# Kernel optimization log

Hardware: AMD Instinct MI355X
Metric: run time of the kernel (lower is better)

The kernel has to match this reference:

```python
import jax, jax.numpy as jnp
import numpy as np
import math

B, L = 2, 768
C, CS, CZ, H, NB = 256, 256, 64, 8, 4
HD = C // H  # 32


def _layernorm(x, g, b):
    mu = jnp.mean(x, -1, keepdims=True)
    var = jnp.var(x, -1, keepdims=True)
    return (x - mu) * jax.lax.rsqrt(var + 1e-5) * g + b


def _adaln(x, cond, g, beta, pw, pb):
    # x: [B,L,C], cond: [B,C] -> LN(x)*(1+scale)+shift
    ss = cond @ pw + pb  # [B, 2C]
    scale, shift = jnp.split(ss, 2, axis=-1)
    return _layernorm(x, g, beta) * (1.0 + scale[:, None, :]) + shift[:, None, :]


def _gelu(x):
    return jax.nn.gelu(x, approximate=False)  # torch nn.GELU default = exact erf


def _axis_angle_to_R(v):
    # Rodrigues: [...,3] -> [...,3,3]
    n = jnp.linalg.norm(v, axis=-1, keepdims=True)
    angle = n[..., None]  # [...,1,1]
    axis = v / (n + 1e-8)
    x, y, z = axis[..., 0], axis[..., 1], axis[..., 2]
    zero = jnp.zeros_like(x)
    K = jnp.stack([
        jnp.stack([zero, -z, y], -1),
        jnp.stack([z, zero, -x], -1),
        jnp.stack([-y, x, zero], -1),
    ], -2)
    eye = jnp.broadcast_to(jnp.eye(3, dtype=v.dtype), K.shape)
    return eye + jnp.sin(angle) * K + (1.0 - jnp.cos(angle)) * (K @ K)


def setup_inputs() -> dict:
    key = jax.random.key(0)
    ks = iter(jax.random.split(key, 64))
    nk = lambda: next(ks)
    w = lambda shape, s=0.02: jax.random.normal(nk(), shape, jnp.float32) * s
    return {
        'rots': jax.random.normal(nk(), (B, L, 3, 3), jnp.float32),
        'trans': jax.random.normal(nk(), (B, L, 3), jnp.float32),
        't': jax.random.uniform(nk(), (B,), jnp.float32),
        'single': jax.random.normal(nk(), (B, L, CS), jnp.float32),
        'pair': jax.random.normal(nk(), (B, L, L, CZ), jnp.float32),
        'frame_w': w((12, C)), 'frame_b': w((C,)),
        'single_w': w((CS, C)), 'single_b': w((C,)),
        'tw1': w((C, 4 * C)), 'tb1': w((4 * C,)),
        'tw2': w((4 * C, C)), 'tb2': w((C,)),
        'out_w': w((C, 6)), 'out_b': w((6,)),
        'ag1': jnp.ones((NB, C)), 'abeta1': jnp.zeros((NB, C)),
        'apw1': w((NB, C, 2 * C)), 'apb1': w((NB, 2 * C)),
        'wq': w((NB, C, C)), 'wk': w((NB, C, C)), 'wv': w((NB, C, C)),
        'pw': w((NB, CZ, H)),
        'wo': w((NB, C, C)), 'wob': w((NB, C)),
        'ag2': jnp.ones((NB, C)), 'abeta2': jnp.zeros((NB, C)),
        'apw2': w((NB, C, 2 * C)), 'apb2': w((NB, 2 * C)),
        'fw1': w((NB, C, 4 * C)), 'fb1': w((NB, 4 * C)),
        'fw2': w((NB, 4 * C, C)), 'fb2': w((NB, C)),
    }


def reference(rots, trans, t, single, pair, frame_w, frame_b, single_w, single_b,
              tw1, tb1, tw2, tb2, out_w, out_b, ag1, abeta1, apw1, apb1,
              wq, wk, wv, pw, wo, wob, ag2, abeta2, apw2, apb2,
              fw1, fb1, fw2, fb2):
    Bq, Lq = trans.shape[:2]
    # frame featurization + single conditioning
    frame_feat = jnp.concatenate([rots.reshape(Bq, Lq, 9), trans], -1)  # [B,L,12]
    h = frame_feat @ frame_w + frame_b + single @ single_w + single_b   # [B,L,C]
    # Fourier time embedding -> MLP
    half = C // 2
    freqs = jnp.exp(-math.log(10000.0) * jnp.arange(half, dtype=jnp.float32) / half)
    args = t[:, None] * freqs
    temb = jnp.concatenate([jnp.cos(args), jnp.sin(args)], -1)          # [B,C]
    time_cond = _gelu(temb @ tw1 + tb1) @ tw2 + tb2                     # [B,C]
    scale = 1.0 / math.sqrt(HD)
    for i in range(NB):
        hh = _adaln(h, time_cond, ag1[i], abeta1[i], apw1[i], apb1[i])
        q = (hh @ wq[i]).reshape(Bq, Lq, H, HD)
        k = (hh @ wk[i]).reshape(Bq, Lq, H, HD)
        v = (hh @ wv[i]).reshape(Bq, Lq, H, HD)
        logits = jnp.einsum('bihd,bjhd->bhij', q, k) * scale
        logits = logits + jnp.einsum('bijc,ch->bhij', pair, pw[i])      # pair bias
        attn = jax.nn.softmax(logits, -1)
        out = jnp.einsum('bhij,bjhd->bihd', attn, v).reshape(Bq, Lq, C)
        h = h + out @ wo[i] + wob[i]
        h2 = _adaln(h, time_cond, ag2[i], abeta2[i], apw2[i], apb2[i])
        h = h + _gelu(h2 @ fw1[i] + fb1[i]) @ fw2[i] + fb2[i]
    corr = h @ out_w + out_b                                            # [B,L,6]
    R_upd = _axis_angle_to_R(corr[..., :3])
    t_upd = corr[..., 3:]
    # compose: new_R = R @ R_upd, new_t = R @ t_upd + t
    new_rots = rots @ R_upd
    new_trans = jnp.einsum('blij,blj->bli', rots, t_upd) + trans
    return jnp.concatenate([new_rots.reshape(Bq, Lq, 9), new_trans], -1)  # [B,L,12]
```

## Files before the change

### kernel.cpp

```cpp
#include <hip/hip_runtime.h>
#include <math.h>

#define BB 2
#define LL 768
#define CC 256
#define CZ 64
#define NH 8
#define NBLK 4
#define HD 32
#define BL (BB*LL)

typedef unsigned short ushort_t;
typedef float f32x4 __attribute__((ext_vector_type(4)));
typedef __bf16 bf16x8 __attribute__((ext_vector_type(8)));

__device__ __forceinline__ float gelu_exact(float x) {
    return 0.5f * x * (1.0f + erff(x * 0.70710678118654752f));
}

__device__ __forceinline__ ushort_t f2bf(float f) {
    union { float f; unsigned u; } x; x.f = f;
    unsigned r = x.u + 0x7fffu + ((x.u >> 16) & 1u);
    return (ushort_t)(r >> 16);
}

__device__ __forceinline__ float bf2f(ushort_t u) {
    union { unsigned u; float f; } x; x.u = ((unsigned)u) << 16;
    return x.f;
}

__global__ __launch_bounds__(512) void k_time_pre(
        const float* __restrict__ t, float* __restrict__ temb,
        float* __restrict__ tmid, float* __restrict__ time_cond) {
    int tid = threadIdx.x;
    int b = tid >> 8, idx = tid & 255;
    int fi = idx & 127;
    float f = expf(-logf(10000.0f) * (float)fi / 128.0f);
    float a = t[b] * f;
    temb[b * 256 + idx] = (idx < 128) ? cosf(a) : sinf(a);
    #pragma unroll
    for (int e = 0; e < 4; ++e) tmid[tid + 512 * e] = 0.f;
    time_cond[tid] = 0.f;
}

__global__ __launch_bounds__(256) void k_time1(
        const float* __restrict__ temb, const float* __restrict__ tw1,
        float* __restrict__ tmid) {
    int kc = blockIdx.x, b = blockIdx.y;
    int tid = threadIdx.x;
    __shared__ float te[32];
    if (tid < 32) te[tid] = temb[b * 256 + kc * 32 + tid];
    __syncthreads();
    float acc[4] = {0.f, 0.f, 0.f, 0.f};
    #pragma unroll
    for (int k = 0; k < 32; ++k) {
        const float* wr = tw1 + (size_t)(kc * 32 + k) * 1024;
        float tv = te[k];
        #pragma unroll
        for (int m = 0; m < 4; ++m) acc[m] += tv * wr[tid + 256 * m];
    }
    #pragma unroll
    for (int m = 0; m < 4; ++m) atomicAdd(&tmid[b * 1024 + tid + 256 * m], acc[m]);
}

__global__ __launch_bounds__(512) void k_time_gelu(
        float* __restrict__ tmid, const float* __restrict__ tb1) {
    int tid = threadIdx.x;
    #pragma unroll
    for (int e = 0; e < 4; ++e) {
        int i = tid + 512 * e;
        tmid[i] = gelu_exact(tmid[i] + tb1[i & 1023]);
    }
}

__global__ __launch_bounds__(256) void k_time2(
        const float* __restrict__ tmid, const float* __restrict__ tw2,
        const float* __restrict__ tb2, float* __restrict__ time_cond) {
    int kc = blockIdx.x, b = blockIdx.y;
    int tid = threadIdx.x;
    __shared__ float mg[64];
    if (tid < 64) mg[tid] = tmid[b * 1024 + kc * 64 + tid];
    __syncthreads();
    float acc = (kc == 0) ? tb2[tid] : 0.f;
    #pragma unroll
    for (int k = 0; k < 64; ++k)
        acc += mg[k] * tw2[(size_t)(kc * 64 + k) * 256 + tid];
    atomicAdd(&time_cond[b * 256 + tid], acc);
}

__global__ __launch_bounds__(512) void k_ss(
        const float* __restrict__ tc,
        const float* __restrict__ apw1, const float* __restrict__ apb1,
        const float* __restrict__ apw2, const float* __restrict__ apb2,
        float* __restrict__ ss1, float* __restrict__ ss2) {
    int n = blockIdx.x, b = blockIdx.y, which = blockIdx.z;
    const float* apw = which ? apw2 : apw1;
    const float* apb = which ? apb2 : apb1;
    float* ss = which ? ss2 : ss1;
    __shared__ float tcl[256];
    int tid = threadIdx.x;
    if (tid < 256) tcl[tid] = tc[b * 256 + tid];
    __syncthreads();
    float acc = apb[n * 512 + tid];
    const float* w = apw + (size_t)n * 256 * 512 + tid;
    #pragma unroll 8
    for (int k = 0; k < 256; ++k) acc += tcl[k] * w[(size_t)k * 512];
    ss[(size_t)(n * BB + b) * 512 + tid] = acc;
}

__global__ __launch_bounds__(256) void k_init_h(
        const float* __restrict__ rots, const float* __restrict__ trans,
        const float* __restrict__ single,
        const float* __restrict__ frame_w, const float* __restrict__ frame_b,
        const float* __restrict__ single_w, const float* __restrict__ single_b,
        float* __restrict__ h) {
    int row = blockIdx.x;
    int tid = threadIdx.x;
    __shared__ float ff[12];
    __shared__ float sr[256];
    if (tid < 9) ff[tid] = rots[(size_t)row * 9 + tid];
    else if (tid < 12) ff[tid] = trans[(size_t)row * 3 + (tid - 9)];
    sr[tid] = single[(size_t)row * 256 + tid];
    __syncthreads();
    float acc = frame_b[tid] + single_b[tid];
    #pragma unroll
    for (int k = 0; k < 12; ++k) acc += ff[k] * frame_w[k * 256 + tid];
    #pragma unroll 8
    for (int k = 0; k < 256; ++k) acc += sr[k] * single_w[k * 256 + tid];
    h[(size_t)row * 256 + tid] = acc;
}

__global__ __launch_bounds__(256) void k_adaln(
        const float* __restrict__ h, const float* __restrict__ g,
        const float* __restrict__ beta, const float* __restrict__ ss,
        float* __restrict__ out) {
    int row = blockIdx.x;
    int b = row / LL;
    int tid = threadIdx.x;
    float x = h[(size_t)row * 256 + tid];
    float s = x, sq = x * x;
    #pragma unroll
    for (int off = 32; off > 0; off >>= 1) {
        s  += __shfl_down(s,  off, 64);
        sq += __shfl_down(sq, off, 64);
    }
    __shared__ float red[8];
    int wave = tid >> 6, lane = tid & 63;
    if (lane == 0) { red[wave] = s; red[4 + wave] = sq; }
    __syncthreads();
    if (tid == 0) {
        float ts = red[0] + red[1] + red[2] + red[3];
        float tq = red[4] + red[5] + red[6] + red[7];
        float mu = ts * (1.0f / 256.0f);
        float var = tq * (1.0f / 256.0f) - mu * mu;
        red[0] = mu;
        red[1] = rsqrtf(var + 1e-5f);
    }
    __syncthreads();
    float mu = red[0], inv = red[1];
    float ln = (x - mu) * inv * g[tid] + beta[tid];
    float scale = ss[b * 512 + tid];
    float shift = ss[b * 512 + 256 + tid];
    out[(size_t)row * 256 + tid] = ln * (1.0f + scale) + shift;
}

__global__ __launch_bounds__(256) void k_adaln_bf(
        const float* __restrict__ h, const float* __restrict__ g,
        const float* __restrict__ beta, const float* __restrict__ ss,
        ushort_t* __restrict__ out) {
    int row = blockIdx.x;
    int b = row / LL;
    int tid = threadIdx.x;
    float x = h[(size_t)row * 256 + tid];
    float s = x, sq = x * x;
    #pragma unroll
    for (int off = 32; off > 0; off >>= 1) {
        s  += __shfl_down(s,  off, 64);
        sq += __shfl_down(sq, off, 64);
    }
    __shared__ float red[8];
    int wave = tid >> 6, lane = tid & 63;
    if (lane == 0) { red[wave] = s; red[4 + wave] = sq; }
    __syncthreads();
    if (tid == 0) {
        float ts = red[0] + red[1] + red[2] + red[3];
        float tq = red[4] + red[5] + red[6] + red[7];
        float mu = ts * (1.0f / 256.0f);
        float var = tq * (1.0f / 256.0f) - mu * mu;
        red[0] = mu;
        red[1] = rsqrtf(var + 1e-5f);
    }
    __syncthreads();
    float mu = red[0], inv = red[1];
    float ln = (x - mu) * inv * g[tid] + beta[tid];
    float scale = ss[b * 512 + tid];
    float shift = ss[b * 512 + 256 + tid];
    out[(size_t)row * 256 + tid] = f2bf(ln * (1.0f + scale) + shift);
}

__global__ __launch_bounds__(256) void k_wt(
        const float* __restrict__ wq, const float* __restrict__ wk,
        const float* __restrict__ wv, const float* __restrict__ wo,
        const float* __restrict__ fw1, const float* __restrict__ fw2,
        ushort_t* __restrict__ wqkv_bt, ushort_t* __restrict__ wo_bt,
        ushort_t* __restrict__ fw1_bt, ushort_t* __restrict__ fw2_bt) {
    int type = blockIdx.z, nb = blockIdx.y, idx = blockIdx.x;
    int K, N; const float* src; ushort_t* dst;
    switch (type) {
        case 0: K = 256; N = 256;  src = wq  + (size_t)nb * 65536;  dst = wqkv_bt + (size_t)nb * 196608;           break;
        case 1: K = 256; N = 256;  src = wk  + (size_t)nb * 65536;  dst = wqkv_bt + (size_t)nb * 196608 + 65536;   break;
        case 2: K = 256; N = 256;  src = wv  + (size_t)nb * 65536;  dst = wqkv_bt + (size_t)nb * 196608 + 131072;  break;
        case 3: K = 256; N = 256;  src = wo  + (size_t)nb * 65536;  dst = wo_bt  + (size_t)nb * 65536;             break;
        case 4: K = 256; N = 1024; src = fw1 + (size_t)nb * 262144; dst = fw1_bt + (size_t)nb * 262144;            break;
        default:K = 1024; N = 256; src = fw2 + (size_t)nb * 262144; dst = fw2_bt + (size_t)nb * 262144;            break;
    }
    int tilesN = N >> 6;
    int tiles = (K >> 6) * tilesN;
    if (idx >= tiles) return;
    int k0 = (idx / tilesN) * 64, n0 = (idx % tilesN) * 64;
    __shared__ float lds[64][65];
    int tn = threadIdx.x & 63, tk = threadIdx.x >> 6;
    #pragma unroll
    for (int r = 0; r < 16; ++r) {
        int kk = tk + 4 * r;
        lds[kk][tn] = src[(size_t)(k0 + kk) * N + n0 + tn];
    }
    __syncthreads();
    #pragma unroll
    for (int r = 0; r < 16; ++r) {
        int nn = tk + 4 * r;
        dst[(size_t)(n0 + nn) * K + k0 + tn] = f2bf(lds[tn][nn]);
    }
}

template<int KSTEPS, int MODE>
__global__ __launch_bounds__(256) void k_mfma(
        const ushort_t* __restrict__ A, const ushort_t* __restrict__ Wt,
        const float* __restrict__ bias, const float* __restrict__ resid,
        float* __restrict__ outf, ushort_t* __restrict__ outb,
        ushort_t* __restrict__ qo, ushort_t* __restrict__ ko,
        ushort_t* __restrict__ vo) {
    const int K = KSTEPS * 32;
    int m0 = blockIdx.x * 64, n0 = blockIdx.y * 64;
    int t = threadIdx.x;
    int wave = t >> 6, lane = t & 63, quad = lane >> 4, l16 = lane & 15;
    const bf16x8* Ap = (const bf16x8*)(A + (size_t)(m0 + wave * 16 + l16) * K + quad * 8);
    const bf16x8* Wp = (const bf16x8*)(Wt + (size_t)(n0 + l16) * K + quad * 8);
    const int wstride = 2 * K;
    f32x4 acc[4];
    #pragma unroll
    for (int nt = 0; nt < 4; ++nt) acc[nt] = f32x4{0.f, 0.f, 0.f, 0.f};

    #pragma unroll
    for (int ks = 0; ks < KSTEPS; ++ks) {
        bf16x8 av = Ap[ks * 4];
        #pragma unroll
        for (int nt = 0; nt < 4; ++nt) {
            bf16x8 bv = Wp[nt * wstride + ks * 4];
            acc[nt] = __builtin_amdgcn_mfma_f32_16x16x32_bf16(av, bv, acc[nt], 0, 0, 0);
        }
    }

    int row_base = m0 + wave * 16 + quad * 4;
    #pragma unroll
    for (int nt = 0; nt < 4; ++nt) {
        int n = n0 + nt * 16 + l16;
        #pragma unroll
        for (int r = 0; r < 4; ++r) {
            int row = row_base + r;
            float val = acc[nt][r];
            if (MODE == 0) {
                if (n < 512) {
                    ushort_t* dst = (n < 256) ? qo : ko;
                    dst[(size_t)row * 256 + (n & 255)] = f2bf(val);
                } else {
                    int d = n & 31, hd = (n >> 5) & 7;
                    int bb = (row >= LL) ? 1 : 0;
                    int i = row - bb * LL;
                    vo[(((size_t)(bb * NH + hd)) * 32 + d) * LL + i] = f2bf(val);
                }
            } else if (MODE == 1) {
                val += bias[n] + resid[(size_t)row * 256 + n];
                outf[(size_t)row * 256 + n] = val;
            } else {
                val = gelu_exact(val + bias[n]);
                outb[(size_t)row * 1024 + n] = f2bf(val);
            }
        }
    }
}

template<int KSTEPS>
__global__ __launch_bounds__(256) void k_mfma32(
        const ushort_t* __restrict__ A, const ushort_t* __restrict__ Wt,
        const float* __restrict__ bias, const float* __restrict__ resid,
        float* __restrict__ outf) {
    const int K = KSTEPS * 32;
    int m0 = blockIdx.x * 32, n0 = blockIdx.y * 32;
    int t = threadIdx.x;
    int wave = t >> 6, lane = t & 63, quad = lane >> 4, l16 = lane & 15;
    int msub = wave & 1, nsub = wave >> 1;
    const bf16x8* Ap = (const bf16x8*)(A + (size_t)(m0 + msub * 16 + l16) * K + quad * 8);
    const bf16x8* Wp = (const bf16x8*)(Wt + (size_t)(n0 + nsub * 16 + l16) * K + quad * 8);
    f32x4 acc = {0.f, 0.f, 0.f, 0.f};
    #pragma unroll 8
    for (int ks = 0; ks < KSTEPS; ++ks)
        acc = __builtin_amdgcn_mfma_f32_16x16x32_bf16(Ap[ks * 4], Wp[ks * 4], acc, 0, 0, 0);
    int n = n0 + nsub * 16 + l16;
    int row0 = m0 + msub * 16 + quad * 4;
    float bv = bias[n];
    #pragma unroll
    for (int r = 0; r < 4; ++r) {
        int row = row0 + r;
        outf[(size_t)row * 256 + n] = acc[r] + bv + resid[(size_t)row * 256 + n];
    }
}

template<int NCOL, int KCH>
__global__ __launch_bounds__(256) void k_gemm4(
        const float* __restrict__ A, const float* __restrict__ W,
        const float* __restrict__ bias, const float* __restrict__ resid,
        float* __restrict__ out, int flags) {
    const int N = 256 * NCOL;
    const int K = 256 * KCH;
    int row0 = blockIdx.x * 4;
    int tid = threadIdx.x;
    __shared__ float a_s[4][256];
    float acc[4][NCOL];
    #pragma unroll
    for (int r = 0; r < 4; ++r)
        #pragma unroll
        for (int m = 0; m < NCOL; ++m) acc[r][m] = 0.f;

    for (int kc = 0; kc < KCH; ++kc) {
        if (kc) __syncthreads();
        {
            int r = tid >> 6, c4 = tid & 63;
            float4 av = reinterpret_cast<const float4*>(
                A + (size_t)(row0 + r) * K + kc * 256)[c4];
            *reinterpret_cast<float4*>(&a_s[r][c4 * 4]) = av;
        }
        __syncthreads();
        const float* Wp = W + (size_t)kc * 256 * N + tid;
        #pragma unroll 4
        for (int k = 0; k < 256; ++k) {
            float bv[NCOL];
            #pragma unroll
            for (int m = 0; m < NCOL; ++m) bv[m] = Wp[(size_t)k * N + 256 * m];
            #pragma unroll
            for (int r = 0; r < 4; ++r) {
                float a = a_s[r][k];
                #pragma unroll
                for (int m = 0; m < NCOL; ++m) acc[r][m] += a * bv[m];
            }
        }
    }
    #pragma unroll
    for (int r = 0; r < 4; ++r) {
        int row = row0 + r;
        #pragma unroll
        for (int m = 0; m < NCOL; ++m) {
            int col = tid + 256 * m;
            float v = acc[r][m];
            if (flags & 1) v += bias[col];
            if (flags & 2) v = gelu_exact(v);
            if (flags & 4) v += resid[(size_t)row * N + col];
            out[(size_t)row * N + col] = v;
        }
    }
}

__global__ __launch_bounds__(256) void k_gemm_qkv(
        const float* __restrict__ A,
        const float* __restrict__ Wq, const float* __restrict__ Wk,
        const float* __restrict__ Wv,
        float* __restrict__ q, float* __restrict__ k_,
        float* __restrict__ v) {
    int row0 = blockIdx.x * 4;
    int tid = threadIdx.x;
    __shared__ float a_s[4][256];
    {
        int r = tid >> 6, c4 = tid & 63;
        float4 av = reinterpret_cast<const float4*>(
            A + (size_t)(row0 + r) * 256)[c4];
        *reinterpret_cast<float4*>(&a_s[r][c4 * 4]) = av;
    }
    __syncthreads();
    float aq[4] = {0,0,0,0}, ak[4] = {0,0,0,0}, av_[4] = {0,0,0,0};
    #pragma unroll 4
    for (int k = 0; k < 256; ++k) {
        float wq_ = Wq[(size_t)k * 256 + tid];
        float wk_ = Wk[(size_t)k * 256 + tid];
        float wv_ = Wv[(size_t)k * 256 + tid];
        #pragma unroll
        for (int r = 0; r < 4; ++r) {
            float a = a_s[r][k];
            aq[r]  += a * wq_;
            ak[r]  += a * wk_;
            av_[r] += a * wv_;
        }
    }
    #pragma unroll
    for (int r = 0; r < 4; ++r) {
        size_t o = (size_t)(row0 + r) * 256 + tid;
        q[o] = aq[r]; k_[o] = ak[r]; v[o] = av_[r];
    }
}

__global__ __launch_bounds__(256) void k_pairbias(
        const float* __restrict__ pair, const float* __restrict__ pw,
        float* __restrict__ pb) {
    int row = blockIdx.x;
    int b = row / LL, i = row % LL;
    int t = threadIdx.x;
    int wave = t >> 6, lane = t & 63, quad = lane >> 4, l16 = lane & 15;

    bf16x8 Bhi[2][2], Blo[2][2];
    #pragma unroll
    for (int tt = 0; tt < 2; ++tt) {
        int nh = tt * 16 + l16;
        int n = nh >> 3, hh = nh & 7;
        #pragma unroll
        for (int ks = 0; ks < 2; ++ks) {
            #pragma unroll
            for (int e = 0; e < 8; ++e) {
                int c = ks * 32 + quad * 8 + e;
                float w = pw[n * 512 + c * 8 + hh];
                __bf16 hi = (__bf16)w;
                float lo = w - (float)hi;
                Bhi[tt][ks][e] = hi;
                Blo[tt][ks][e] = (__bf16)lo;
            }
        }
    }

    const float* prow = pair + (size_t)row * LL * CZ;
    for (int x = 0; x < 12; ++x) {
        int j0 = (wave + 4 * x) * 16;
        bf16x8 Ahi[2], Alo[2];
        #pragma unroll
        for (int ks = 0; ks < 2; ++ks) {
            const float4* src = reinterpret_cast<const float4*>(
                prow + (size_t)(j0 + l16) * CZ + ks * 32 + quad * 8);
            float4 v0 = src[0], v1 = src[1];
            float f[8] = {v0.x, v0.y, v0.z, v0.w, v1.x, v1.y, v1.z, v1.w};
            #pragma unroll
            for (int e = 0; e < 8; ++e) {
                __bf16 hi = (__bf16)f[e];
                Ahi[ks][e] = hi;
                Alo[ks][e] = (__bf16)(f[e] - (float)hi);
            }
        }
        #pragma unroll
        for (int tt = 0; tt < 2; ++tt) {
            f32x4 acc = {0.f, 0.f, 0.f, 0.f};
            #pragma unroll
            for (int ks = 0; ks < 2; ++ks) {
                acc = __builtin_amdgcn_mfma_f32_16x16x32_bf16(Ahi[ks], Bhi[tt][ks], acc, 0, 0, 0);
                acc = __builtin_amdgcn_mfma_f32_16x16x32_bf16(Alo[ks], Bhi[tt][ks], acc, 0, 0, 0);
                acc = __builtin_amdgcn_mfma_f32_16x16x32_bf16(Ahi[ks], Blo[tt][ks], acc, 0, 0, 0);
            }
            int nh = tt * 16 + l16;
            float4 o = make_float4(acc[0], acc[1], acc[2], acc[3]);
            *reinterpret_cast<float4*>(
                pb + (((size_t)(b * 32 + nh)) * LL + i) * LL + j0 + quad * 4) = o;
        }
    }
}

__global__ __launch_bounds__(256) void k_attn_mfma(
        const ushort_t* __restrict__ qb, const ushort_t* __restrict__ kb,
        const ushort_t* __restrict__ vt, const float* __restrict__ pb,
        int n, ushort_t* __restrict__ outp) {
    int it = blockIdx.x, h = blockIdx.y, b = blockIdx.z;
    int i0 = it * 32;
    int t = threadIdx.x;
    int wave = t >> 6, lane = t & 63, quad = lane >> 4, l16 = lane & 15;
    int qsub = wave & 1, jhalf = wave >> 1;

    __shared__ __align__(16) ushort_t Plds[4][2][16][40];
    __shared__ float mbuf[2][2][16];
    __shared__ float lbuf[2][2][16];
    __shared__ float obuf[2][2][16][33];

    bf16x8 qfrag = *(const bf16x8*)(
        qb + ((size_t)(b * LL + i0 + qsub * 16 + l16)) * 256 + h * 32 + quad * 8);

    f32x4 O0 = {0.f,0.f,0.f,0.f}, O1 = {0.f,0.f,0.f,0.f};
    float mr[4] = {-1e30f,-1e30f,-1e30f,-1e30f};
    float lr[4] = {0.f,0.f,0.f,0.f};

    const float scale = 0.17677669529663687f;
    const int jbase = jhalf * 384;
    const ushort_t* kp = kb + ((size_t)(b * LL + jbase)) * 256 + h * 32 + quad * 8;
    const ushort_t* vp = vt + (((size_t)(b * NH + h)) * 32 + l16) * LL + jbase + quad * 8;
    const float* pbp = pb
        + (((size_t)(b * 32 + n * NH + h)) * LL + (i0 + qsub * 16 + quad * 4)) * LL
        + jbase + l16;

    for (int jt = 0; jt < 12; ++jt) {
        int j0 = jt * 32;
        bf16x8 kf0 = *(const bf16x8*)(kp + (size_t)(j0 + l16) * 256);
        bf16x8 kf1 = *(const bf16x8*)(kp + (size_t)(j0 + 16 + l16) * 256);
        f32x4 s0 = __builtin_amdgcn_mfma_f32_16x16x32_bf16(qfrag, kf0, (f32x4){0.f,0.f,0.f,0.f}, 0, 0, 0);
        f32x4 s1 = __builtin_amdgcn_mfma_f32_16x16x32_bf16(qfrag, kf1, (f32x4){0.f,0.f,0.f,0.f}, 0, 0, 0);
        #pragma unroll
        for (int r = 0; r < 4; ++r) {
            float b0 = pbp[(size_t)r * LL + j0];
            float b1 = pbp[(size_t)r * LL + j0 + 16];
            s0[r] = s0[r] * scale + b0;
            s1[r] = s1[r] * scale + b1;
        }
        float tmax[4];
        #pragma unroll
        for (int r = 0; r < 4; ++r) tmax[r] = fmaxf(s0[r], s1[r]);
        #pragma unroll
        for (int mk = 1; mk <= 8; mk <<= 1) {
            #pragma unroll
            for (int r = 0; r < 4; ++r)
                tmax[r] = fmaxf(tmax[r], __shfl_xor(tmax[r], mk, 64));
        }
        #pragma unroll
        for (int r = 0; r < 4; ++r) {
            float mn = fmaxf(mr[r], tmax[r]);
            float c = __expf(mr[r] - mn);
            mr[r] = mn;
            lr[r] *= c;
            O0[r] *= c;
            O1[r] *= c;
        }
        float p0[4], p1[4], rs[4];
        #pragma unroll
        for (int r = 0; r < 4; ++r) {
            p0[r] = __expf(s0[r] - mr[r]);
            p1[r] = __expf(s1[r] - mr[r]);
            rs[r] = p0[r] + p1[r];
        }
        #pragma unroll
        for (int mk = 1; mk <= 8; mk <<= 1) {
            #pragma unroll
            for (int r = 0; r < 4; ++r)
                rs[r] += __shfl_xor(rs[r], mk, 64);
        }
        #pragma unroll
        for (int r = 0; r < 4; ++r) lr[r] += rs[r];
        #pragma unroll
        for (int r = 0; r < 4; ++r) {
            int qr = quad * 4 + r;
            ushort_t h0 = f2bf(p0[r]);
            ushort_t h1 = f2bf(p1[r]);
            Plds[wave][0][qr][l16]      = h0;
            Plds[wave][0][qr][16 + l16] = h1;
            Plds[wave][1][qr][l16]      = f2bf(p0[r] - bf2f(h0));
            Plds[wave][1][qr][16 + l16] = f2bf(p1[r] - bf2f(h1));
        }
        asm volatile("" ::: "memory");
        bf16x8 pfh = *(const bf16x8*)&Plds[wave][0][l16][quad * 8];
        bf16x8 pfl = *(const bf16x8*)&Plds[wave][1][l16][quad * 8];
        asm volatile("" ::: "memory");
        bf16x8 vf0 = *(const bf16x8*)(vp + j0);
        bf16x8 vf1 = *(const bf16x8*)(vp + (size_t)16 * LL + j0);
        O0 = __builtin_amdgcn_mfma_f32_16x16x32_bf16(pfh, vf0, O0, 0, 0, 0);
        O0 = __builtin_amdgcn_mfma_f32_16x16x32_bf16(pfl, vf0, O0, 0, 0, 0);
        O1 = __builtin_amdgcn_mfma_f32_16x16x32_bf16(pfh, vf1, O1, 0, 0, 0);
        O1 = __builtin_amdgcn_mfma_f32_16x16x32_bf16(pfl, vf1, O1, 0, 0, 0);
    }

    if (l16 == 0) {
        #pragma unroll
        for (int r = 0; r < 4; ++r) {
            mbuf[qsub][jhalf][quad * 4 + r] = mr[r];
            lbuf[qsub][jhalf][quad * 4 + r] = lr[r];
        }
    }
    #pragma unroll
    for (int r = 0; r < 4; ++r) {
        obuf[qsub][jhalf][quad * 4 + r][l16]      = O0[r];
        obuf[qsub][jhalf][quad * 4 + r][16 + l16] = O1[r];
    }
    __syncthreads();

    {
        int q = t >> 3;
        int qs = q >> 4, ql = q & 15;
        int d0 = (t & 7) * 4;
        float m0 = mbuf[qs][0][ql], m1 = mbuf[qs][1][ql];
        float M = fmaxf(m0, m1);
        float w0 = __expf(m0 - M), w1 = __expf(m1 - M);
        float lt = lbuf[qs][0][ql] * w0 + lbuf[qs][1][ql] * w1;
        float inv = 1.0f / lt;
        ushort4 o4;
        o4.x = f2bf((obuf[qs][0][ql][d0+0]*w0 + obuf[qs][1][ql][d0+0]*w1) * inv);
        o4.y = f2bf((obuf[qs][0][ql][d0+1]*w0 + obuf[qs][1][ql][d0+1]*w1) * inv);
        o4.z = f2bf((obuf[qs][0][ql][d0+2]*w0 + obuf[qs][1][ql][d0+2]*w1) * inv);
        o4.w = f2bf((obuf[qs][0][ql][d0+3]*w0 + obuf[qs][1][ql][d0+3]*w1) * inv);
        *reinterpret_cast<ushort4*>(
            outp + ((size_t)(b * LL + i0 + q)) * 256 + h * 32 + d0) = o4;
    }
}

__global__ __launch_bounds__(256) void k_attn(
        const float* __restrict__ q, const float* __restrict__ kk,
        const float* __restrict__ v, const float* __restrict__ pair,
        const float* __restrict__ pw, float* __restrict__ outp) {
    int blk = blockIdx.x;
    int b = blk / LL, i = blk % LL;
    int tid = threadIdx.x;
    __shared__ float q_s[256];
    __shared__ float pw_s[CZ * NH];
    __shared__ float lg[NH][LL];
    __shared__ float part[8][256];
    __shared__ float invs[NH];
    size_t rowq = (size_t)(b * LL + i) * 256;
    q_s[tid] = q[rowq + tid];
    pw_s[tid] = pw[tid];
    pw_s[tid + 256] = pw[tid + 256];
    __syncthreads();

    const float scale = 0.17677669529663687f;
    for (int j = tid; j < LL; j += 256) {
        const float4* k4 = reinterpret_cast<const float4*>(kk + (size_t)(b * LL + j) * 256);
        const float4* q4 = reinterpret_cast<const float4*>(q_s);
        float dot[NH];
        #pragma unroll
        for (int h = 0; h < NH; ++h) {
            float sx = 0.f, sy = 0.f, sz = 0.f, sw = 0.f;
            #pragma unroll
            for (int dd = 0; dd < 8; ++dd) {
                float4 kv = k4[h * 8 + dd];
                float4 qv = q4[h * 8 + dd];
                sx += qv.x * kv.x; sy += qv.y * kv.y;
                sz += qv.z * kv.z; sw += qv.w * kv.w;
            }
            dot[h] = (sx + sy) + (sz + sw);
        }
        const float4* p4 = reinterpret_cast<const float4*>(
            pair + ((size_t)(b * LL + i) * LL + j) * CZ);
        float bias[NH];
        #pragma unroll
        for (int h = 0; h < NH; ++h) bias[h] = 0.f;
        #pragma unroll
        for (int c4 = 0; c4 < 16; ++c4) {
            float4 pv = p4[c4];
            int c = c4 * 4;
            #pragma unroll
            for (int h = 0; h < NH; ++h)
                bias[h] += pv.x * pw_s[(c + 0) * NH + h] + pv.y * pw_s[(c + 1) * NH + h]
                         + pv.z * pw_s[(c + 2) * NH + h] + pv.w * pw_s[(c + 3) * NH + h];
        }
        #pragma unroll
        for (int h = 0; h < NH; ++h) lg[h][j] = dot[h] * scale + bias[h];
    }
    __syncthreads();

    int wave = tid >> 6, lane = tid & 63;
    for (int h = wave; h < NH; h += 4) {
        float mx = -1e30f;
        for (int j = lane; j < LL; j += 64) mx = fmaxf(mx, lg[h][j]);
        #pragma unroll
        for (int off = 32; off > 0; off >>= 1) mx = fmaxf(mx, __shfl_xor(mx, off, 64));
        float sm = 0.f;
        for (int j = lane; j < LL; j += 64) {
            float e = __expf(lg[h][j] - mx);
            lg[h][j] = e;
            sm += e;
        }
        #pragma unroll
        for (int off = 32; off > 0; off >>= 1) sm += __shfl_xor(sm, off, 64);
        if (lane == 0) invs[h] = 1.0f / sm;
    }
    __syncthreads();

    int g = tid >> 5, d = tid & 31;
    float acc[NH];
    #pragma unroll
    for (int h = 0; h < NH; ++h) acc[h] = 0.f;
    for (int j = g; j < LL; j += 8) {
        const float* vr = v + (size_t)(b * LL + j) * 256;
        #pragma unroll
        for (int h = 0; h < NH; ++h) acc[h] += lg[h][j] * vr[h * 32 + d];
    }
    #pragma unroll
    for (int h = 0; h < NH; ++h) part[g][h * 32 + d] = acc[h];
    __syncthreads();
    float sum = 0.f;
    #pragma unroll
    for (int g2 = 0; g2 < 8; ++g2) sum += part[g2][tid];
    outp[rowq + tid] = sum * invs[tid >> 5];
}

__global__ __launch_bounds__(256) void k_final(
        const float* __restrict__ h, const float* __restrict__ out_w,
        const float* __restrict__ out_b, const float* __restrict__ rots,
        const float* __restrict__ trans, float* __restrict__ out) {
    __shared__ float w_s[256 * 6];
    int t = threadIdx.x, wave = t >> 6, lane = t & 63;
    for (int i = t; i < 1536; i += 256) w_s[i] = out_w[i];
    __syncthreads();
    int row = blockIdx.x * 4 + wave;
    const float* hr = h + (size_t)row * 256;
    float4 hv = reinterpret_cast<const float4*>(hr)[lane];
    int k0 = lane * 4;
    float c[6];
    #pragma unroll
    for (int cc = 0; cc < 6; ++cc)
        c[cc] = hv.x * w_s[(k0+0)*6+cc] + hv.y * w_s[(k0+1)*6+cc]
              + hv.z * w_s[(k0+2)*6+cc] + hv.w * w_s[(k0+3)*6+cc];
    #pragma unroll
    for (int off = 32; off > 0; off >>= 1)
        #pragma unroll
        for (int cc = 0; cc < 6; ++cc)
            c[cc] += __shfl_xor(c[cc], off, 64);
    if (lane == 0) {
        float corr[6];
        #pragma unroll
        for (int cc = 0; cc < 6; ++cc) corr[cc] = c[cc] + out_b[cc];
        float vx = corr[0], vy = corr[1], vz = corr[2];
        float n = sqrtf(vx * vx + vy * vy + vz * vz);
        float inv = 1.0f / (n + 1e-8f);
        float ax = vx * inv, ay = vy * inv, az = vz * inv;
        float s = sinf(n), ccs = 1.0f - cosf(n);
        float K[9] = {0.f, -az, ay,  az, 0.f, -ax,  -ay, ax, 0.f};
        float K2[9];
        #pragma unroll
        for (int ii = 0; ii < 3; ++ii)
            #pragma unroll
            for (int jj = 0; jj < 3; ++jj)
                K2[ii * 3 + jj] = K[ii * 3 + 0] * K[0 * 3 + jj]
                                + K[ii * 3 + 1] * K[1 * 3 + jj]
                                + K[ii * 3 + 2] * K[2 * 3 + jj];
        float R[9];
        #pragma unroll
        for (int ii = 0; ii < 3; ++ii)
            #pragma unroll
            for (int jj = 0; jj < 3; ++jj)
                R[ii * 3 + jj] = (ii == jj ? 1.0f : 0.0f) + s * K[ii * 3 + jj] + ccs * K2[ii * 3 + jj];
        const float* ro = rots + (size_t)row * 9;
        float* o = out + (size_t)row * 12;
        #pragma unroll
        for (int ii = 0; ii < 3; ++ii)
            #pragma unroll
            for (int jj = 0; jj < 3; ++jj)
                o[ii * 3 + jj] = ro[ii * 3 + 0] * R[0 * 3 + jj]
                               + ro[ii * 3 + 1] * R[1 * 3 + jj]
                               + ro[ii * 3 + 2] * R[2 * 3 + jj];
        float t0 = corr[3], t1 = corr[4], t2 = corr[5];
        const float* tr = trans + (size_t)row * 3;
        #pragma unroll
        for (int ii = 0; ii < 3; ++ii)
            o[9 + ii] = ro[ii * 3 + 0] * t0 + ro[ii * 3 + 1] * t1 + ro[ii * 3 + 2] * t2 + tr[ii];
    }
}

extern "C" void kernel_launch(void* const* d_in, const int* in_sizes, int n_in,
                              void* d_out, int out_size, void* d_ws, size_t ws_size,
                              hipStream_t stream) {
    (void)in_sizes; (void)n_in; (void)out_size;
    const float* rots     = (const float*)d_in[0];
    const float* trans    = (const float*)d_in[1];
    const float* t        = (const float*)d_in[2];
    const float* single   = (const float*)d_in[3];
    const float* pair     = (const float*)d_in[4];
    const float* frame_w  = (const float*)d_in[5];
    const float* frame_b  = (const float*)d_in[6];
    const float* single_w = (const float*)d_in[7];
    const float* single_b = (const float*)d_in[8];
    const float* tw1      = (const float*)d_in[9];
    const float* tb1      = (const float*)d_in[10];
    const float* tw2      = (const float*)d_in[11];
    const float* tb2      = (const float*)d_in[12];
    const float* out_w    = (const float*)d_in[13];
    const float* out_b    = (const float*)d_in[14];
    const float* ag1      = (const float*)d_in[15];
    const float* abeta1   = (const float*)d_in[16];
    const float* apw1     = (const float*)d_in[17];
    const float* apb1     = (const float*)d_in[18];
    const float* wq       = (const float*)d_in[19];
    const float* wk       = (const float*)d_in[20];
    const float* wv       = (const float*)d_in[21];
    const float* pw       = (const float*)d_in[22];
    const float* wo       = (const float*)d_in[23];
    const float* wob      = (const float*)d_in[24];
    const float* ag2      = (const float*)d_in[25];
    const float* abeta2   = (const float*)d_in[26];
    const float* apw2     = (const float*)d_in[27];
    const float* apb2     = (const float*)d_in[28];
    const float* fw1      = (const float*)d_in[29];
    const float* fb1      = (const float*)d_in[30];
    const float* fw2      = (const float*)d_in[31];
    const float* fb2      = (const float*)d_in[32];

    float* ws = (float*)d_ws;
    float* time_cond = ws;
    float* ss1 = time_cond + 512;
    float* ss2 = ss1 + 4096;
    float* h   = ss2 + 4096;
    float* hh  = h + 393216;
    float* q   = hh + 393216;
    float* k_  = q + 393216;
    float* v   = k_ + 393216;
    float* attnout = v + 393216;
    float* mid = attnout + 393216;
    float* pb  = mid + 1572864;

    float* tmid    = mid;
    float* temb_ws = mid + 2048;

    const size_t base_floats = 3940864ull;
    const size_t pb_floats = 37748736ull;
    ushort_t* us = (ushort_t*)(ws + base_floats + pb_floats);
    ushort_t* hh_bf      = us;
    ushort_t* attnout_bf = hh_bf + 393216;
    ushort_t* mid_bf     = attnout_bf + 393216;
    ushort_t* wqkv_bt    = mid_bf + 1572864;
    ushort_t* wo_bt      = wqkv_bt + 786432;
    ushort_t* fw1_bt     = wo_bt + 262144;
    ushort_t* fw2_bt     = fw1_bt + 1048576;
    const size_t us_count = 5505024ull;

    ushort_t* qb  = (ushort_t*)q;
    ushort_t* kbb = (ushort_t*)k_;
    ushort_t* vtb = (ushort_t*)v;

    const size_t need = (base_floats + pb_floats) * 4ull + us_count * 2ull;
    const bool big = ws_size >= need;

    k_time_pre<<<1, 512, 0, stream>>>(t, temb_ws, tmid, time_cond);
    k_time1<<<dim3(8, BB), 256, 0, stream>>>(temb_ws, tw1, tmid);
    k_time_gelu<<<1, 512, 0, stream>>>(tmid, tb1);
    k_time2<<<dim3(16, BB), 256, 0, stream>>>(tmid, tw2, tb2, time_cond);
    k_ss<<<dim3(NBLK, BB, 2), 512, 0, stream>>>(time_cond, apw1, apb1, apw2, apb2, ss1, ss2);
    k_init_h<<<BL, 256, 0, stream>>>(rots, trans, single, frame_w, frame_b,
                                     single_w, single_b, h);
    if (big) {
        k_wt<<<dim3(64, NBLK, 6), 256, 0, stream>>>(wq, wk, wv, wo, fw1, fw2,
                                                    wqkv_bt, wo_bt, fw1_bt, fw2_bt);
        k_pairbias<<<BL, 256, 0, stream>>>(pair, pw, pb);
        for (int n = 0; n < NBLK; ++n) {
            k_adaln_bf<<<BL, 256, 0, stream>>>(h, ag1 + n * 256, abeta1 + n * 256,
                                               ss1 + (size_t)n * BB * 512, hh_bf);
            k_mfma<8, 0><<<dim3(24, 12), 256, 0, stream>>>(
                hh_bf, wqkv_bt + (size_t)n * 196608, nullptr, nullptr,
                nullptr, nullptr, qb, kbb, vtb);
            k_attn_mfma<<<dim3(24, NH, BB), 256, 0, stream>>>(
                qb, kbb, vtb, pb, n, attnout_bf);
            k_mfma32<8><<<dim3(48, 8), 256, 0, stream>>>(
                attnout_bf, wo_bt + (size_t)n * 65536, wob + n * 256, h, h);
            k_adaln_bf<<<BL, 256, 0, stream>>>(h, ag2 + n * 256, abeta2 + n * 256,
                                               ss2 + (size_t)n * BB * 512, hh_bf);
            k_mfma<8, 2><<<dim3(24, 16), 256, 0, stream>>>(
                hh_bf, fw1_bt + (size_t)n * 262144, fb1 + n * 1024, nullptr,
                nullptr, mid_bf, nullptr, nullptr, nullptr);
            k_mfma32<32><<<dim3(48, 8), 256, 0, stream>>>(
                mid_bf, fw2_bt + (size_t)n * 262144, fb2 + n * 256, h, h);
        }
    } else {
        for (int n = 0; n < NBLK; ++n) {
            k_adaln<<<BL, 256, 0, stream>>>(h, ag1 + n * 256, abeta1 + n * 256,
                                            ss1 + (size_t)n * BB * 512, hh);
            k_gemm_qkv<<<BL / 4, 256, 0, stream>>>(hh, wq + (size_t)n * 65536,
                                                   wk + (size_t)n * 65536,
                                                   wv + (size_t)n * 65536, q, k_, v);
            k_attn<<<BL, 256, 0, stream>>>(q, k_, v, pair, pw + n * 512, attnout);
            k_gemm4<1, 1><<<BL / 4, 256, 0, stream>>>(attnout, wo + (size_t)n * 65536,
                                                      wob + n * 256, h, h, 1 | 4);
            k_adaln<<<BL, 256, 0, stream>>>(h, ag2 + n * 256, abeta2 + n * 256,
                                            ss2 + (size_t)n * BB * 512, hh);
            k_gemm4<4, 1><<<BL / 4, 256, 0, stream>>>(hh, fw1 + (size_t)n * 262144,
                                                      fb1 + n * 1024, nullptr, mid, 1 | 2);
            k_gemm4<1, 4><<<BL / 4, 256, 0, stream>>>(mid, fw2 + (size_t)n * 262144,
                                                      fb2 + n * 256, h, h, 1 | 4);
        }
    }
    k_final<<<BL / 4, 256, 0, stream>>>(h, out_w, out_b, rots, trans, (float*)d_out);
}
```

Measured before the change: 884.7 us.

## Store pair bias in bf16, stage GEMM outputs via LDS, rebalance attention

The precomputed pair-bias tensor is now stored as bf16 instead of fp32, with writes staged through a shared tile so they are coalesced. This halves the largest memory stream that attention reads. The QKV and FFN GEMM epilogues also go through an LDS tile and write 16-byte vectors, including the transposed V. Attention now uses 16 query rows per block with four waves splitting the keys, which doubles the grid. Several time-embedding kernels are fused and the ss projection is split along K with atomics, at the cost of bf16 rounding in the bias and extra syncs.

```diff
diff --git a/kernel.cpp b/kernel.cpp
--- a/kernel.cpp
+++ b/kernel.cpp
@@ -13,6 +13,7 @@
 typedef unsigned short ushort_t;
 typedef float f32x4 __attribute__((ext_vector_type(4)));
 typedef __bf16 bf16x8 __attribute__((ext_vector_type(8)));
+typedef ushort_t us8 __attribute__((ext_vector_type(8)));
 
 __device__ __forceinline__ float gelu_exact(float x) {
     return 0.5f * x * (1.0f + erff(x * 0.70710678118654752f));
@@ -29,27 +30,33 @@
     return x.f;
 }
 
-__global__ __launch_bounds__(512) void k_time_pre(
-        const float* __restrict__ t, float* __restrict__ temb,
-        float* __restrict__ tmid, float* __restrict__ time_cond) {
+__global__ __launch_bounds__(512) void k_zero(
+        float* __restrict__ tmid, float* __restrict__ time_cond,
+        float* __restrict__ ss1, float* __restrict__ ss2) {
     int tid = threadIdx.x;
-    int b = tid >> 8, idx = tid & 255;
-    int fi = idx & 127;
-    float f = expf(-logf(10000.0f) * (float)fi / 128.0f);
-    float a = t[b] * f;
-    temb[b * 256 + idx] = (idx < 128) ? cosf(a) : sinf(a);
     #pragma unroll
     for (int e = 0; e < 4; ++e) tmid[tid + 512 * e] = 0.f;
     time_cond[tid] = 0.f;
+    #pragma unroll
+    for (int e = 0; e < 8; ++e) {
+        ss1[tid + 512 * e] = 0.f;
+        ss2[tid + 512 * e] = 0.f;
+    }
 }
 
 __global__ __launch_bounds__(256) void k_time1(
-        const float* __restrict__ temb, const float* __restrict__ tw1,
+        const float* __restrict__ t, const float* __restrict__ tw1,
         float* __restrict__ tmid) {
     int kc = blockIdx.x, b = blockIdx.y;
     int tid = threadIdx.x;
     __shared__ float te[32];
-    if (tid < 32) te[tid] = temb[b * 256 + kc * 32 + tid];
+    if (tid < 32) {
+        int idx = kc * 32 + tid;
+        int fi = idx & 127;
+        float f = expf(-logf(10000.0f) * (float)fi / 128.0f);
+        float a = t[b] * f;
+        te[tid] = (idx < 128) ? cosf(a) : sinf(a);
+    }
     __syncthreads();
     float acc[4] = {0.f, 0.f, 0.f, 0.f};
     #pragma unroll
@@ -63,23 +70,17 @@
     for (int m = 0; m < 4; ++m) atomicAdd(&tmid[b * 1024 + tid + 256 * m], acc[m]);
 }
 
-__global__ __launch_bounds__(512) void k_time_gelu(
-        float* __restrict__ tmid, const float* __restrict__ tb1) {
-    int tid = threadIdx.x;
-    #pragma unroll
-    for (int e = 0; e < 4; ++e) {
-        int i = tid + 512 * e;
-        tmid[i] = gelu_exact(tmid[i] + tb1[i & 1023]);
-    }
-}
-
 __global__ __launch_bounds__(256) void k_time2(
-        const float* __restrict__ tmid, const float* __restrict__ tw2,
-        const float* __restrict__ tb2, float* __restrict__ time_cond) {
+        const float* __restrict__ tmid, const float* __restrict__ tb1,
+        const float* __restrict__ tw2, const float* __restrict__ tb2,
+        float* __restrict__ time_cond) {
     int kc = blockIdx.x, b = blockIdx.y;
     int tid = threadIdx.x;
     __shared__ float mg[64];
-    if (tid < 64) mg[tid] = tmid[b * 1024 + kc * 64 + tid];
+    if (tid < 64) {
+        int idx = kc * 64 + tid;
+        mg[tid] = gelu_exact(tmid[b * 1024 + idx] + tb1[idx]);
+    }
     __syncthreads();
     float acc = (kc == 0) ? tb2[tid] : 0.f;
     #pragma unroll
@@ -93,19 +94,20 @@
         const float* __restrict__ apw1, const float* __restrict__ apb1,
         const float* __restrict__ apw2, const float* __restrict__ apb2,
         float* __restrict__ ss1, float* __restrict__ ss2) {
-    int n = blockIdx.x, b = blockIdx.y, which = blockIdx.z;
+    int kc = blockIdx.x & 7, n = blockIdx.x >> 3;
+    int b = blockIdx.y, which = blockIdx.z;
     const float* apw = which ? apw2 : apw1;
     const float* apb = which ? apb2 : apb1;
     float* ss = which ? ss2 : ss1;
-    __shared__ float tcl[256];
+    __shared__ float tcl[32];
     int tid = threadIdx.x;
-    if (tid < 256) tcl[tid] = tc[b * 256 + tid];
-    __syncthreads();
-    float acc = apb[n * 512 + tid];
-    const float* w = apw + (size_t)n * 256 * 512 + tid;
+    if (tid < 32) tcl[tid] = tc[b * 256 + kc * 32 + tid];
+    __syncthreads();
+    float acc = (kc == 0) ? apb[n * 512 + tid] : 0.f;
+    const float* w = apw + (size_t)n * 256 * 512 + (size_t)(kc * 32) * 512 + tid;
     #pragma unroll 8
-    for (int k = 0; k < 256; ++k) acc += tcl[k] * w[(size_t)k * 512];
-    ss[(size_t)(n * BB + b) * 512 + tid] = acc;
+    for (int k = 0; k < 32; ++k) acc += tcl[k] * w[(size_t)k * 512];
+    atomicAdd(&ss[(size_t)(n * BB + b) * 512 + tid], acc);
 }
 
 __global__ __launch_bounds__(256) void k_init_h(
@@ -236,14 +238,14 @@
 template<int KSTEPS, int MODE>
 __global__ __launch_bounds__(256) void k_mfma(
         const ushort_t* __restrict__ A, const ushort_t* __restrict__ Wt,
-        const float* __restrict__ bias, const float* __restrict__ resid,
-        float* __restrict__ outf, ushort_t* __restrict__ outb,
+        const float* __restrict__ bias, ushort_t* __restrict__ outb,
         ushort_t* __restrict__ qo, ushort_t* __restrict__ ko,
         ushort_t* __restrict__ vo) {
     const int K = KSTEPS * 32;
     int m0 = blockIdx.x * 64, n0 = blockIdx.y * 64;
     int t = threadIdx.x;
     int wave = t >> 6, lane = t & 63, quad = lane >> 4, l16 = lane & 15;
+    __shared__ ushort_t ot[64][72];
     const bf16x8* Ap = (const bf16x8*)(A + (size_t)(m0 + wave * 16 + l16) * K + quad * 8);
     const bf16x8* Wp = (const bf16x8*)(Wt + (size_t)(n0 + l16) * K + quad * 8);
     const int wstride = 2 * K;
@@ -261,32 +263,48 @@
         }
     }
 
-    int row_base = m0 + wave * 16 + quad * 4;
+    int row_l = wave * 16 + quad * 4;
     #pragma unroll
     for (int nt = 0; nt < 4; ++nt) {
-        int n = n0 + nt * 16 + l16;
+        int col = nt * 16 + l16;
         #pragma unroll
         for (int r = 0; r < 4; ++r) {
-            int row = row_base + r;
             float val = acc[nt][r];
-            if (MODE == 0) {
-                if (n < 512) {
-                    ushort_t* dst = (n < 256) ? qo : ko;
-                    dst[(size_t)row * 256 + (n & 255)] = f2bf(val);
-                } else {
-                    int d = n & 31, hd = (n >> 5) & 7;
-                    int bb = (row >= LL) ? 1 : 0;
-                    int i = row - bb * LL;
-                    vo[(((size_t)(bb * NH + hd)) * 32 + d) * LL + i] = f2bf(val);
-                }
-            } else if (MODE == 1) {
-                val += bias[n] + resid[(size_t)row * 256 + n];
-                outf[(size_t)row * 256 + n] = val;
-            } else {
-                val = gelu_exact(val + bias[n]);
-                outb[(size_t)row * 1024 + n] = f2bf(val);
-            }
-        }
+            if (MODE == 2) val = gelu_exact(val + bias[n0 + col]);
+            ot[row_l + r][col] = f2bf(val);
+        }
+    }
+    __syncthreads();
+
+    if (MODE == 2) {
+        int rr = t >> 2, cc = (t & 3) * 16;
+        us8 v0 = *(const us8*)&ot[rr][cc];
+        us8 v1 = *(const us8*)&ot[rr][cc + 8];
+        size_t o = (size_t)(m0 + rr) * 1024 + n0 + cc;
+        *(us8*)&outb[o] = v0;
+        *(us8*)&outb[o + 8] = v1;
+    } else if (n0 < 512) {
+        ushort_t* dst = (n0 < 256) ? qo : ko;
+        int rr = t >> 2, cc = (t & 3) * 16;
+        us8 v0 = *(const us8*)&ot[rr][cc];
+        us8 v1 = *(const us8*)&ot[rr][cc + 8];
+        size_t o = (size_t)(m0 + rr) * 256 + (n0 & 255) + cc;
+        *(us8*)&dst[o] = v0;
+        *(us8*)&dst[o + 8] = v1;
+    } else {
+        int dl = t >> 2, ii = (t & 3) * 16;
+        int ng = n0 + dl;
+        int hd = (ng >> 5) & 7, d = ng & 31;
+        int bb = (m0 >= LL) ? 1 : 0;
+        int ibase = m0 - bb * LL + ii;
+        us8 v0, v1;
+        #pragma unroll
+        for (int e = 0; e < 8; ++e) v0[e] = ot[ii + e][dl];
+        #pragma unroll
+        for (int e = 0; e < 8; ++e) v1[e] = ot[ii + 8 + e][dl];
+        size_t o = (((size_t)(bb * NH + hd)) * 32 + d) * LL + ibase;
+        *(us8*)&vo[o] = v0;
+        *(us8*)&vo[o + 8] = v1;
     }
 }
 
@@ -409,11 +427,13 @@
 
 __global__ __launch_bounds__(256) void k_pairbias(
         const float* __restrict__ pair, const float* __restrict__ pw,
-        float* __restrict__ pb) {
+        ushort_t* __restrict__ pb) {
     int row = blockIdx.x;
     int b = row / LL, i = row % LL;
     int t = threadIdx.x;
     int wave = t >> 6, lane = t & 63, quad = lane >> 4, l16 = lane & 15;
+
+    __shared__ ushort_t tile[32][72];
 
     bf16x8 Bhi[2][2], Blo[2][2];
     #pragma unroll
@@ -435,8 +455,9 @@
     }
 
     const float* prow = pair + (size_t)row * LL * CZ;
+    int wnh = t >> 3, wjj = (t & 7) * 8;
     for (int x = 0; x < 12; ++x) {
-        int j0 = (wave + 4 * x) * 16;
+        int j0 = (4 * x + wave) * 16;
         bf16x8 Ahi[2], Alo[2];
         #pragma unroll
         for (int ks = 0; ks < 2; ++ks) {
@@ -461,44 +482,51 @@
                 acc = __builtin_amdgcn_mfma_f32_16x16x32_bf16(Ahi[ks], Blo[tt][ks], acc, 0, 0, 0);
             }
             int nh = tt * 16 + l16;
-            float4 o = make_float4(acc[0], acc[1], acc[2], acc[3]);
-            *reinterpret_cast<float4*>(
-                pb + (((size_t)(b * 32 + nh)) * LL + i) * LL + j0 + quad * 4) = o;
-        }
+            int jl = wave * 16 + quad * 4;
+            ushort4 st;
+            st.x = f2bf(acc[0]); st.y = f2bf(acc[1]);
+            st.z = f2bf(acc[2]); st.w = f2bf(acc[3]);
+            *reinterpret_cast<ushort4*>(&tile[nh][jl]) = st;
+        }
+        __syncthreads();
+        {
+            us8 v = *(const us8*)&tile[wnh][wjj];
+            *(us8*)&pb[(((size_t)(b * 32 + wnh)) * LL + i) * LL + 64 * x + wjj] = v;
+        }
+        __syncthreads();
     }
 }
 
 __global__ __launch_bounds__(256) void k_attn_mfma(
         const ushort_t* __restrict__ qb, const ushort_t* __restrict__ kb,
-        const ushort_t* __restrict__ vt, const float* __restrict__ pb,
+        const ushort_t* __restrict__ vt, const ushort_t* __restrict__ pb,
         int n, ushort_t* __restrict__ outp) {
     int it = blockIdx.x, h = blockIdx.y, b = blockIdx.z;
-    int i0 = it * 32;
+    int i0 = it * 16;
     int t = threadIdx.x;
     int wave = t >> 6, lane = t & 63, quad = lane >> 4, l16 = lane & 15;
-    int qsub = wave & 1, jhalf = wave >> 1;
 
     __shared__ __align__(16) ushort_t Plds[4][2][16][40];
-    __shared__ float mbuf[2][2][16];
-    __shared__ float lbuf[2][2][16];
-    __shared__ float obuf[2][2][16][33];
+    __shared__ float mbuf[4][16];
+    __shared__ float lbuf[4][16];
+    __shared__ float obuf[4][16][33];
 
     bf16x8 qfrag = *(const bf16x8*)(
-        qb + ((size_t)(b * LL + i0 + qsub * 16 + l16)) * 256 + h * 32 + quad * 8);
+        qb + ((size_t)(b * LL + i0 + l16)) * 256 + h * 32 + quad * 8);
 
     f32x4 O0 = {0.f,0.f,0.f,0.f}, O1 = {0.f,0.f,0.f,0.f};
     float mr[4] = {-1e30f,-1e30f,-1e30f,-1e30f};
     float lr[4] = {0.f,0.f,0.f,0.f};
 
     const float scale = 0.17677669529663687f;
-    const int jbase = jhalf * 384;
+    const int jbase = wave * 192;
     const ushort_t* kp = kb + ((size_t)(b * LL + jbase)) * 256 + h * 32 + quad * 8;
     const ushort_t* vp = vt + (((size_t)(b * NH + h)) * 32 + l16) * LL + jbase + quad * 8;
-    const float* pbp = pb
-        + (((size_t)(b * 32 + n * NH + h)) * LL + (i0 + qsub * 16 + quad * 4)) * LL
+    const ushort_t* pbp = pb
+        + (((size_t)(b * 32 + n * NH + h)) * LL + (i0 + quad * 4)) * LL
         + jbase + l16;
 
-    for (int jt = 0; jt < 12; ++jt) {
+    for (int jt = 0; jt < 6; ++jt) {
         int j0 = jt * 32;
         bf16x8 kf0 = *(const bf16x8*)(kp + (size_t)(j0 + l16) * 256);
         bf16x8 kf1 = *(const bf16x8*)(kp + (size_t)(j0 + 16 + l16) * 256);
@@ -506,8 +534,8 @@
         f32x4 s1 = __builtin_amdgcn_mfma_f32_16x16x32_bf16(qfrag, kf1, (f32x4){0.f,0.f,0.f,0.f}, 0, 0, 0);
         #pragma unroll
         for (int r = 0; r < 4; ++r) {
-            float b0 = pbp[(size_t)r * LL + j0];
-            float b1 = pbp[(size_t)r * LL + j0 + 16];
+            float b0 = bf2f(pbp[(size_t)r * LL + j0]);
+            float b1 = bf2f(pbp[(size_t)r * LL + j0 + 16]);
             s0[r] = s0[r] * scale + b0;
             s1[r] = s1[r] * scale + b1;
         }
@@ -569,33 +597,35 @@
     if (l16 == 0) {
         #pragma unroll
         for (int r = 0; r < 4; ++r) {
-            mbuf[qsub][jhalf][quad * 4 + r] = mr[r];
-            lbuf[qsub][jhalf][quad * 4 + r] = lr[r];
+            mbuf[wave][quad * 4 + r] = mr[r];
+            lbuf[wave][quad * 4 + r] = lr[r];
         }
     }
     #pragma unroll
     for (int r = 0; r < 4; ++r) {
-        obuf[qsub][jhalf][quad * 4 + r][l16]      = O0[r];
-        obuf[qsub][jhalf][quad * 4 + r][16 + l16] = O1[r];
+        obuf[wave][quad * 4 + r][l16]      = O0[r];
+        obuf[wave][quad * 4 + r][16 + l16] = O1[r];
     }
     __syncthreads();
 
     {
-        int q = t >> 3;
-        int qs = q >> 4, ql = q & 15;
-        int d0 = (t & 7) * 4;
-        float m0 = mbuf[qs][0][ql], m1 = mbuf[qs][1][ql];
-        float M = fmaxf(m0, m1);
+        int q = t >> 4;
+        int d0 = (t & 15) * 2;
+        float m0 = mbuf[0][q], m1 = mbuf[1][q], m2 = mbuf[2][q], m3 = mbuf[3][q];
+        float M = fmaxf(fmaxf(m0, m1), fmaxf(m2, m3));
         float w0 = __expf(m0 - M), w1 = __expf(m1 - M);
-        float lt = lbuf[qs][0][ql] * w0 + lbuf[qs][1][ql] * w1;
+        float w2 = __expf(m2 - M), w3 = __expf(m3 - M);
+        float lt = lbuf[0][q] * w0 + lbuf[1][q] * w1 + lbuf[2][q] * w2 + lbuf[3][q] * w3;
         float inv = 1.0f / lt;
-        ushort4 o4;
-        o4.x = f2bf((obuf[qs][0][ql][d0+0]*w0 + obuf[qs][1][ql][d0+0]*w1) * inv);
-        o4.y = f2bf((obuf[qs][0][ql][d0+1]*w0 + obuf[qs][1][ql][d0+1]*w1) * inv);
-        o4.z = f2bf((obuf[qs][0][ql][d0+2]*w0 + obuf[qs][1][ql][d0+2]*w1) * inv);
-        o4.w = f2bf((obuf[qs][0][ql][d0+3]*w0 + obuf[qs][1][ql][d0+3]*w1) * inv);
-        *reinterpret_cast<ushort4*>(
-            outp + ((size_t)(b * LL + i0 + q)) * 256 + h * 32 + d0) = o4;
+        float oa = obuf[0][q][d0] * w0 + obuf[1][q][d0] * w1
+                 + obuf[2][q][d0] * w2 + obuf[3][q][d0] * w3;
+        float ob = obuf[0][q][d0+1] * w0 + obuf[1][q][d0+1] * w1
+                 + obuf[2][q][d0+1] * w2 + obuf[3][q][d0+1] * w3;
+        ushort2 st;
+        st.x = f2bf(oa * inv);
+        st.y = f2bf(ob * inv);
+        *reinterpret_cast<ushort2*>(
+            outp + ((size_t)(b * LL + i0 + q)) * 256 + h * 32 + d0) = st;
     }
 }
 
@@ -801,10 +831,9 @@
     float* v   = k_ + 393216;
     float* attnout = v + 393216;
     float* mid = attnout + 393216;
-    float* pb  = mid + 1572864;
+    float* pbf = mid + 1572864;
 
     float* tmid    = mid;
-    float* temb_ws = mid + 2048;
 
     const size_t base_floats = 3940864ull;
     const size_t pb_floats = 37748736ull;
@@ -818,39 +847,39 @@
     ushort_t* fw2_bt     = fw1_bt + 1048576;
     const size_t us_count = 5505024ull;
 
-    ushort_t* qb  = (ushort_t*)q;
-    ushort_t* kbb = (ushort_t*)k_;
-    ushort_t* vtb = (ushort_t*)v;
+    ushort_t* qb    = (ushort_t*)q;
+    ushort_t* kbb   = (ushort_t*)k_;
+    ushort_t* vtb   = (ushort_t*)v;
+    ushort_t* pb_bf = (ushort_t*)pbf;
 
     const size_t need = (base_floats + pb_floats) * 4ull + us_count * 2ull;
     const bool big = ws_size >= need;
 
-    k_time_pre<<<1, 512, 0, stream>>>(t, temb_ws, tmid, time_cond);
-    k_time1<<<dim3(8, BB), 256, 0, stream>>>(temb_ws, tw1, tmid);
-    k_time_gelu<<<1, 512, 0, stream>>>(tmid, tb1);
-    k_time2<<<dim3(16, BB), 256, 0, stream>>>(tmid, tw2, tb2, time_cond);
-    k_ss<<<dim3(NBLK, BB, 2), 512, 0, stream>>>(time_cond, apw1, apb1, apw2, apb2, ss1, ss2);
+    k_zero<<<1, 512, 0, stream>>>(tmid, time_cond, ss1, ss2);
+    k_time1<<<dim3(8, BB), 256, 0, stream>>>(t, tw1, tmid);
+    k_time2<<<dim3(16, BB), 256, 0, stream>>>(tmid, tb1, tw2, tb2, time_cond);
+    k_ss<<<dim3(32, BB, 2), 512, 0, stream>>>(time_cond, apw1, apb1, apw2, apb2, ss1, ss2);
     k_init_h<<<BL, 256, 0, stream>>>(rots, trans, single, frame_w, frame_b,
                                      single_w, single_b, h);
     if (big) {
         k_wt<<<dim3(64, NBLK, 6), 256, 0, stream>>>(wq, wk, wv, wo, fw1, fw2,
                                                     wqkv_bt, wo_bt, fw1_bt, fw2_bt);
-        k_pairbias<<<BL, 256, 0, stream>>>(pair, pw, pb);
+        k_pairbias<<<BL, 256, 0, stream>>>(pair, pw, pb_bf);
         for (int n = 0; n < NBLK; ++n) {
             k_adaln_bf<<<BL, 256, 0, stream>>>(h, ag1 + n * 256, abeta1 + n * 256,
                                                ss1 + (size_t)n * BB * 512, hh_bf);
             k_mfma<8, 0><<<dim3(24, 12), 256, 0, stream>>>(
-                hh_bf, wqkv_bt + (size_t)n * 196608, nullptr, nullptr,
-                nullptr, nullptr, qb, kbb, vtb);
-            k_attn_mfma<<<dim3(24, NH, BB), 256, 0, stream>>>(
-                qb, kbb, vtb, pb, n, attnout_bf);
+                hh_bf, wqkv_bt + (size_t)n * 196608, nullptr,
+                nullptr, qb, kbb, vtb);
+            k_attn_mfma<<<dim3(48, NH, BB), 256, 0, stream>>>(
+                qb, kbb, vtb, pb_bf, n, attnout_bf);
             k_mfma32<8><<<dim3(48, 8), 256, 0, stream>>>(
                 attnout_bf, wo_bt + (size_t)n * 65536, wob + n * 256, h, h);
             k_adaln_bf<<<BL, 256, 0, stream>>>(h, ag2 + n * 256, abeta2 + n * 256,
                                                ss2 + (size_t)n * BB * 512, hh_bf);
             k_mfma<8, 2><<<dim3(24, 16), 256, 0, stream>>>(
-                hh_bf, fw1_bt + (size_t)n * 262144, fb1 + n * 1024, nullptr,
-                nullptr, mid_bf, nullptr, nullptr, nullptr);
+                hh_bf, fw1_bt + (size_t)n * 262144, fb1 + n * 1024,
+                mid_bf, nullptr, nullptr, nullptr);
             k_mfma32<32><<<dim3(48, 8), 256, 0, stream>>>(
                 mid_bf, fw2_bt + (size_t)n * 262144, fb2 + n * 256, h, h);
         }
```

Result: faster. 807.7 us (-8.7%).
